# Kernel tuning notes

Hardware: AMD Instinct MI355X
Metric: run time of the kernel (lower is better)

## Reference

```python
import jax, jax.numpy as jnp
import numpy as np

N_HEADS = 16


def setup_inputs() -> dict:
    key = jax.random.key(0)
    k1, k2, k3 = jax.random.split(key, 3)
    B, S, D = 2, 2048, 1024
    x = jax.random.normal(k1, (B, S, D), dtype=jnp.float32)
    # causal mask: 1 = keep, 0 = masked (module does masked_fill(mask == 0, -inf))
    mask = jnp.broadcast_to(jnp.tril(jnp.ones((S, S), dtype=jnp.int32)), (B, S, S))
    # torch Linear(bias=False) weights, stored transposed so y = x @ W
    w_qkv = jax.random.normal(k2, (D, 3 * D), dtype=jnp.float32) * (1.0 / np.sqrt(D))
    w_out = jax.random.normal(k3, (D, D), dtype=jnp.float32) * (1.0 / np.sqrt(D))
    return {"x": x, "mask": mask, "w_qkv": w_qkv, "w_out": w_out}


def reference(x, mask, w_qkv, w_out):
    B, S, D = x.shape
    H = N_HEADS
    dh = D // H
    scale = 1.0 / np.sqrt(dh)

    qkv = x @ w_qkv                                   # [B,S,3D]
    qkv = qkv.reshape(B, S, 3, H, dh)
    qkv = jnp.transpose(qkv, (2, 0, 3, 1, 4))         # [3,B,H,S,dh]
    q, k, v = qkv[0], qkv[1], qkv[2]

    scores = jnp.einsum("bhqd,bhkd->bhqk", q, k) * scale   # [B,H,S,S]
    scores = jnp.where(mask[:, None, :, :] == 0, -jnp.inf, scores)
    attn = jax.nn.softmax(scores, axis=-1)            # dropout = identity (eval)

    out = jnp.einsum("bhqk,bhkd->bhqd", attn, v)      # [B,H,S,dh]
    out = jnp.transpose(out, (0, 2, 1, 3)).reshape(B, S, D)
    return out @ w_out
```

## Files before the change

### kernel.cpp

```cpp
#include <hip/hip_runtime.h>

typedef unsigned short u16;
typedef unsigned int u32;
typedef u16 u16x8 __attribute__((ext_vector_type(8)));
typedef u16 u16x4 __attribute__((ext_vector_type(4)));
typedef u32 u32x4 __attribute__((ext_vector_type(4)));
typedef __bf16 bf16x8 __attribute__((ext_vector_type(8)));
typedef float f32x4 __attribute__((ext_vector_type(4)));
typedef float f32x16 __attribute__((ext_vector_type(16)));


static __device__ __forceinline__ u16 bf16_rn(float f) {
    union { float f; u32 u; } a; a.f = f;
    u32 u = a.u;
    return (u16)((u + 0x7FFFu + ((u >> 16) & 1u)) >> 16);
}

static __device__ __forceinline__ bf16x8 as_bf(u16x8 v) {
    return __builtin_bit_cast(bf16x8, v);
}

static __device__ __forceinline__ u32 cvt_pk_bf16(float lo, float hi) {
    u32 r;
    asm("v_cvt_pk_bf16_f32 %0, %1, %2" : "=v"(r) : "v"(lo), "v"(hi));
    return r;
}

static __device__ __forceinline__ void glds16(const u16* g, u16* lds) {
    __builtin_amdgcn_global_load_lds(
        (const __attribute__((address_space(1))) void*)g,
        (__attribute__((address_space(3))) void*)lds, 16, 0, 0);
}


__global__ void k_cvt(const float* __restrict__ src, u16* __restrict__ dst, int n8) {
    int i = blockIdx.x * blockDim.x + threadIdx.x;
    if (i >= n8) return;
    const float4* s = (const float4*)src + (size_t)i * 2;
    float4 a = s[0], b = s[1];
    u16x8 v;
    v[0] = bf16_rn(a.x); v[1] = bf16_rn(a.y); v[2] = bf16_rn(a.z); v[3] = bf16_rn(a.w);
    v[4] = bf16_rn(b.x); v[5] = bf16_rn(b.y); v[6] = bf16_rn(b.z); v[7] = bf16_rn(b.w);
    *(u16x8*)(dst + (size_t)i * 8) = v;
}


__global__ void k_tr_cvt(const float* __restrict__ src, u16* __restrict__ dst,
                         int R, int C) {
    __shared__ float t[32][33];
    const int bx = blockIdx.x * 32, by = blockIdx.y * 32;
    const int tx = threadIdx.x, ty = threadIdx.y;
#pragma unroll
    for (int j = 0; j < 32; j += 8)
        t[ty + j][tx] = src[(size_t)(by + ty + j) * C + bx + tx];
    __syncthreads();
#pragma unroll
    for (int j = 0; j < 32; j += 8)
        dst[(size_t)(bx + ty + j) * R + by + tx] = bf16_rn(t[tx][ty + j]);
}


template <int MODE>
__launch_bounds__(256, 2)
__global__ void k_gemm(const u16* __restrict__ A, const u16* __restrict__ Bt,
                       void* __restrict__ outp, int M, int N, int K) {
    __shared__ __align__(16) u16 As[2][128 * 32];
    __shared__ __align__(16) u16 Bs[2][128 * 32];
    const int tid = threadIdx.x;
    const int l = tid & 63, wv = tid >> 6;
    const int wr = wv >> 1, wc = wv & 1;
    const int l15 = l & 15, lg = l >> 4;
    const int m0 = blockIdx.y * 128, n0 = blockIdx.x * 128;
    const int NT = K >> 5;

    const f32x4 fzero = {0.f, 0.f, 0.f, 0.f};
    f32x4 acc[4][4];
#pragma unroll
    for (int m = 0; m < 4; m++)
#pragma unroll
        for (int n = 0; n < 4; n++) acc[m][n] = fzero;

    const int grow0 = wv * 32 + (l >> 2);
    const int gcol = (l & 3) * 8;

    auto stage = [&](int buf, int kt) {
        const size_t ko = (size_t)kt * 32 + gcol;
        glds16(A  + (size_t)(m0 + grow0) * K + ko,      &As[buf][wv * 1024]);
        glds16(A  + (size_t)(m0 + grow0 + 16) * K + ko, &As[buf][wv * 1024 + 512]);
        glds16(Bt + (size_t)(n0 + grow0) * K + ko,      &Bs[buf][wv * 1024]);
        glds16(Bt + (size_t)(n0 + grow0 + 16) * K + ko, &Bs[buf][wv * 1024 + 512]);
    };

    stage(0, 0);
    int cur = 0;
    for (int kt = 0; kt < NT; ++kt) {
        if (kt + 1 < NT) {
            stage(cur ^ 1, kt + 1);
            asm volatile("s_waitcnt vmcnt(4)" ::: "memory");
        } else {
            asm volatile("s_waitcnt vmcnt(0)" ::: "memory");
        }
        __builtin_amdgcn_s_barrier();
        u16x8 af[4], bfv[4];
#pragma unroll
        for (int m = 0; m < 4; m++)
            af[m] = *(const u16x8*)(&As[cur][(wr * 64 + m * 16 + l15) * 32 + lg * 8]);
#pragma unroll
        for (int n = 0; n < 4; n++)
            bfv[n] = *(const u16x8*)(&Bs[cur][(wc * 64 + n * 16 + l15) * 32 + lg * 8]);
#pragma unroll
        for (int m = 0; m < 4; m++)
#pragma unroll
            for (int n = 0; n < 4; n++)
                acc[m][n] = __builtin_amdgcn_mfma_f32_16x16x32_bf16(
                    as_bf(af[m]), as_bf(bfv[n]), acc[m][n], 0, 0, 0);
        __builtin_amdgcn_s_barrier();
        cur ^= 1;
    }

    if (MODE == 0) {
        u16* qkv = (u16*)outp;
#pragma unroll
        for (int m = 0; m < 4; m++) {
            const int rb = m0 + wr * 64 + m * 16 + lg * 4;
#pragma unroll
            for (int n = 0; n < 4; n++) {
                const int c = n0 + wc * 64 + n * 16;
                const int t = c >> 10, h = (c >> 6) & 15, d0 = (c & 63) + l15;
                const float scl = (t == 0) ? 0.18033688011112042f : 1.0f;
#pragma unroll
                for (int i = 0; i < 4; i++) {
                    const int r = rb + i;
                    const int b = r >> 11, s = r & 2047;
                    qkv[((((size_t)t * 2 + b) * 16 + h) * 2048 + s) * 64 + d0] =
                        bf16_rn(acc[m][n][i] * scl);
                }
            }
        }
    } else {
        float* O = (float*)outp;
#pragma unroll
        for (int m = 0; m < 4; m++) {
            const int rb = m0 + wr * 64 + m * 16 + lg * 4;
#pragma unroll
            for (int n = 0; n < 4; n++) {
                const int c = n0 + wc * 64 + n * 16 + l15;
#pragma unroll
                for (int i = 0; i < 4; i++)
                    O[(size_t)(rb + i) * N + c] = acc[m][n][i];
            }
        }
    }
}


__launch_bounds__(256, 3)
__global__ void k_attn(const u16* __restrict__ qkv, u16* __restrict__ ab) {
    __shared__ __align__(16) char arena[4][9216];
    __shared__ float MLs[4][64];
    const int tid = threadIdx.x, l = tid & 63, wv = tid >> 6;
    const int q = l & 31, h = l >> 5;
    const int bid = blockIdx.x;
    const int bh = bid & 31;
    const int pp = bid >> 5;
    const int b = bh >> 4, hd = bh & 15;
    const size_t plane = (size_t)2048 * 64;
    const u16* Qg = qkv + ((size_t)(0 + b) * 16 + hd) * plane;
    const u16* Kg = qkv + ((size_t)(2 + b) * 16 + hd) * plane;
    const u16* Vg = qkv + ((size_t)(4 + b) * 16 + hd) * plane;
    u16* VT = (u16*)arena[wv];

    const int g = l & 7, qd = l >> 3;
    const u16* Kbase = Kg + (size_t)q * 64 + 8 * h;
    const u16* Vbase = Vg + (size_t)(8 * qd) * 64 + 8 * g;
    const int Fq0 = 8 * (q >> 3) + ((q & 7) ^ ((q >> 3) & 7));
    const int d1 = q + 32;
    const int Fq1 = 8 * (d1 >> 3) + ((d1 & 7) ^ ((d1 >> 3) & 7));
    const u16* vr0 = VT + Fq0 * 72 + 8 * h;
    const u16* vr1 = VT + Fq1 * 72 + 8 * h;
    const float FIXM = 12.0f;

    for (int ph = 0; ph < 4; ++ph) {
        const int pr = (ph & 2) ? pp + 16 : pp;
        const int qt = (ph & 1) ? 63 - pr : pr;
        const int q0 = qt * 32, qg = q0 + q;
        const int n64 = (qt >> 1) + 1;

        u16x8 qf[4];
#pragma unroll
        for (int s = 0; s < 4; ++s)
            qf[s] = *(const u16x8*)(Qg + (size_t)(q0 + q) * 64 + s * 16 + 8 * h);

        f32x16 oacc0 = 0, oacc1 = 0;
        float l_run = 0.f;

        u16x8 vK[8];
        if (wv < n64) {
#pragma unroll
            for (int s = 0; s < 4; ++s) {
                vK[s]     = *(const u16x8*)(Kbase + (size_t)(wv * 64) * 64 + s * 16);
                vK[4 + s] = *(const u16x8*)(Kbase + (size_t)(wv * 64 + 32) * 64 + s * 16);
            }
        }

        for (int t = wv; t < n64; t += 4) {
            const int kv0 = t * 64;
            u16x8 vV[8];
#pragma unroll
            for (int j = 0; j < 8; ++j)
                vV[j] = *(const u16x8*)(Vbase + (size_t)(kv0 + j) * 64);
            f32x16 sa = 0, sb = 0;
            __builtin_amdgcn_s_setprio(1);
#pragma unroll
            for (int s = 0; s < 4; ++s)
                sa = __builtin_amdgcn_mfma_f32_32x32x16_bf16(as_bf(vK[s]), as_bf(qf[s]), sa, 0, 0, 0);
#pragma unroll
            for (int s = 0; s < 4; ++s)
                sb = __builtin_amdgcn_mfma_f32_32x32x16_bf16(as_bf(vK[4 + s]), as_bf(qf[s]), sb, 0, 0, 0);
            __builtin_amdgcn_s_setprio(0);
#pragma unroll
            for (int j = 0; j < 8; ++j) {
                u16x8 col;
#pragma unroll
                for (int r = 0; r < 8; ++r) col[r] = vV[r][j];
                *(u16x8*)(VT + (size_t)(8 * g + (j ^ g)) * 72 + 8 * qd) = col;
            }
            if (t + 4 < n64) {
#pragma unroll
                for (int s = 0; s < 4; ++s) {
                    vK[s]     = *(const u16x8*)(Kbase + (size_t)((t + 4) * 64) * 64 + s * 16);
                    vK[4 + s] = *(const u16x8*)(Kbase + (size_t)((t + 4) * 64 + 32) * 64 + s * 16);
                }
            }
            if (t == n64 - 1) {
#pragma unroll
                for (int r = 0; r < 16; ++r) {
                    const int kg = kv0 + (r & 3) + 8 * (r >> 2) + 4 * h;
                    if (kg > qg) sa[r] = -__builtin_inff();
                    if (kg + 32 > qg) sb[r] = -__builtin_inff();
                }
            }
#pragma unroll
            for (int r = 0; r < 16; ++r) sa[r] = exp2f(sa[r] - FIXM);
#pragma unroll
            for (int r = 0; r < 16; ++r) sb[r] = exp2f(sb[r] - FIXM);
            float ts[8];
#pragma unroll
            for (int i = 0; i < 8; ++i)
                ts[i] = (sa[i] + sa[i + 8]) + (sb[i] + sb[i + 8]);
#pragma unroll
            for (int i = 0; i < 4; ++i) ts[i] += ts[i + 4];
            l_run += (ts[0] + ts[2]) + (ts[1] + ts[3]);
            u32 pk[16];
#pragma unroll
            for (int i = 0; i < 8; ++i) pk[i]     = cvt_pk_bf16(sa[2 * i], sa[2 * i + 1]);
#pragma unroll
            for (int i = 0; i < 8; ++i) pk[8 + i] = cvt_pk_bf16(sb[2 * i], sb[2 * i + 1]);
#pragma unroll
            for (int ks = 0; ks < 4; ++ks) {
                const int base = (ks >> 1) * 8 + 4 * (ks & 1);
                const u32 o0 = pk[base], o1 = pk[base + 1], o2 = pk[base + 2], o3 = pk[base + 3];
                const u32 sd0 = h ? o0 : o2, sd1 = h ? o1 : o3;
                const u32 r0 = (u32)__shfl_xor((int)sd0, 32);
                const u32 r1 = (u32)__shfl_xor((int)sd1, 32);
                const u32 w0 = h ? r0 : o0, w1 = h ? r1 : o1;
                const u32 w2 = h ? o2 : r0, w3 = h ? o3 : r1;
                const u16x8 pb = __builtin_bit_cast(u16x8, (u32x4){w0, w1, w2, w3});
                const u16x8 va0 = *(const u16x8*)(vr0 + ks * 16);
                const u16x8 va1 = *(const u16x8*)(vr1 + ks * 16);
                __builtin_amdgcn_s_setprio(1);
                oacc0 = __builtin_amdgcn_mfma_f32_32x32x16_bf16(as_bf(va0), as_bf(pb), oacc0, 0, 0, 0);
                oacc1 = __builtin_amdgcn_mfma_f32_32x32x16_bf16(as_bf(va1), as_bf(pb), oacc1, 0, 0, 0);
                __builtin_amdgcn_s_setprio(0);
            }
        }
        asm volatile("" ::: "memory");
        float* Op = (float*)arena[wv];
#pragma unroll
        for (int r = 0; r < 16; ++r) {
            const int dr = (r & 3) + 8 * (r >> 2) + 4 * h;
            Op[q * 64 + ((dr + 2 * q) & 63)]      = oacc0[r];
            Op[q * 64 + ((dr + 32 + 2 * q) & 63)] = oacc1[r];
        }
        MLs[wv][l] = l_run;
        __syncthreads();
        const int tq = tid >> 3, dblk = (tid & 7) * 8;
        float L = 0.f;
#pragma unroll
        for (int w = 0; w < 4; ++w) L += MLs[w][tq] + MLs[w][32 + tq];
        const float inv = 1.f / L;
        u16x8 outv;
#pragma unroll
        for (int j = 0; j < 8; ++j) {
            const int d = dblk + j;
            float acc = 0.f;
#pragma unroll
            for (int w = 0; w < 4; ++w)
                acc += ((const float*)arena[w])[tq * 64 + ((d + 2 * tq) & 63)];
            outv[j] = bf16_rn(acc * inv);
        }
        *(u16x8*)(ab + (size_t)(b * 2048 + q0 + tq) * 1024 + hd * 64 + dblk) = outv;
        __syncthreads();
    }
}


extern "C" void kernel_launch(void* const* d_in, const int* in_sizes, int n_in,
                              void* d_out, int out_size, void* d_ws, size_t ws_size,
                              hipStream_t stream) {
    const float* x     = (const float*)d_in[0];
    const float* w_qkv = (const float*)d_in[2];
    const float* w_out = (const float*)d_in[3];
    float* out = (float*)d_out;
    u16* ws = (u16*)d_ws;

    u16* xb    = ws;
    u16* wqkvT = ws + 4194304;
    u16* woutT = ws + 7340032;
    u16* qkvb  = ws + 8388608;
    u16* abuf  = ws;

    k_cvt<<<2048, 256, 0, stream>>>(x, xb, 524288);
    k_tr_cvt<<<dim3(96, 32), dim3(32, 8), 0, stream>>>(w_qkv, wqkvT, 1024, 3072);
    k_tr_cvt<<<dim3(32, 32), dim3(32, 8), 0, stream>>>(w_out, woutT, 1024, 1024);
    k_gemm<0><<<dim3(24, 32), 256, 0, stream>>>(xb, wqkvT, qkvb, 4096, 3072, 1024);
    k_attn<<<512, 256, 0, stream>>>(qkvb, abuf);
    k_gemm<1><<<dim3(8, 32), 256, 0, stream>>>(abuf, woutT, out, 4096, 1024, 1024);
}
```

Before: 133.9 us.

## Split attention KV tile into two 32-key halves to interleave softmax and MFMA

The inner attention loop now processes each 64-key tile as two 32-key halves. It computes scores, exp, bf16 packing and the PV MFMAs for the first half before issuing the QK MFMAs for the second half. V transposes and the K prefetch loads are also split and spread across the halves. The aim is to cut peak register pressure and let exp and conversion work overlap with matrix instructions. The risk is more serialized dependencies within a wave, plus extra half-width LDS writes.

Result: no change. 136.0 us (+1.6%).

```diff
diff --git a/kernel.cpp b/kernel.cpp
--- a/kernel.cpp
+++ b/kernel.cpp
@@ -205,61 +205,61 @@
 
         for (int t = wv; t < n64; t += 4) {
             const int kv0 = t * 64;
-            u16x8 vV[8];
-#pragma unroll
-            for (int j = 0; j < 8; ++j)
-                vV[j] = *(const u16x8*)(Vbase + (size_t)(kv0 + j) * 64);
-            f32x16 sa = 0, sb = 0;
+            const bool diag = (t == n64 - 1);
+            const bool more = (t + 4 < n64);
+            u16x4 cA[4];
+            u16x8 vVa[4];
+#pragma unroll
+            for (int j = 0; j < 4; ++j)
+                vVa[j] = *(const u16x8*)(Vbase + (size_t)(kv0 + j) * 64);
+            f32x16 sa = 0;
             __builtin_amdgcn_s_setprio(1);
 #pragma unroll
             for (int s = 0; s < 4; ++s)
                 sa = __builtin_amdgcn_mfma_f32_32x32x16_bf16(as_bf(vK[s]), as_bf(qf[s]), sa, 0, 0, 0);
-#pragma unroll
-            for (int s = 0; s < 4; ++s)
-                sb = __builtin_amdgcn_mfma_f32_32x32x16_bf16(as_bf(vK[4 + s]), as_bf(qf[s]), sb, 0, 0, 0);
             __builtin_amdgcn_s_setprio(0);
+            u16x8 vVb[4];
+#pragma unroll
+            for (int j = 0; j < 4; ++j)
+                vVb[j] = *(const u16x8*)(Vbase + (size_t)(kv0 + 4 + j) * 64);
 #pragma unroll
             for (int j = 0; j < 8; ++j) {
-                u16x8 col;
-#pragma unroll
-                for (int r = 0; r < 8; ++r) col[r] = vV[r][j];
-                *(u16x8*)(VT + (size_t)(8 * g + (j ^ g)) * 72 + 8 * qd) = col;
-            }
-            if (t + 4 < n64) {
-#pragma unroll
-                for (int s = 0; s < 4; ++s) {
-                    vK[s]     = *(const u16x8*)(Kbase + (size_t)((t + 4) * 64) * 64 + s * 16);
-                    vK[4 + s] = *(const u16x8*)(Kbase + (size_t)((t + 4) * 64 + 32) * 64 + s * 16);
-                }
-            }
-            if (t == n64 - 1) {
+                u16x4 col = { vVa[0][j], vVa[1][j], vVa[2][j], vVa[3][j] };
+                *(u16x4*)(VT + (size_t)(8 * g + (j ^ g)) * 72 + 8 * qd) = col;
+            }
+            if (diag) {
 #pragma unroll
                 for (int r = 0; r < 16; ++r) {
                     const int kg = kv0 + (r & 3) + 8 * (r >> 2) + 4 * h;
                     if (kg > qg) sa[r] = -__builtin_inff();
-                    if (kg + 32 > qg) sb[r] = -__builtin_inff();
                 }
             }
 #pragma unroll
             for (int r = 0; r < 16; ++r) sa[r] = exp2f(sa[r] - FIXM);
-#pragma unroll
-            for (int r = 0; r < 16; ++r) sb[r] = exp2f(sb[r] - FIXM);
-            float ts[8];
-#pragma unroll
-            for (int i = 0; i < 8; ++i)
-                ts[i] = (sa[i] + sa[i + 8]) + (sb[i] + sb[i + 8]);
-#pragma unroll
-            for (int i = 0; i < 4; ++i) ts[i] += ts[i + 4];
-            l_run += (ts[0] + ts[2]) + (ts[1] + ts[3]);
-            u32 pk[16];
-#pragma unroll
-            for (int i = 0; i < 8; ++i) pk[i]     = cvt_pk_bf16(sa[2 * i], sa[2 * i + 1]);
-#pragma unroll
-            for (int i = 0; i < 8; ++i) pk[8 + i] = cvt_pk_bf16(sb[2 * i], sb[2 * i + 1]);
-#pragma unroll
-            for (int ks = 0; ks < 4; ++ks) {
-                const int base = (ks >> 1) * 8 + 4 * (ks & 1);
-                const u32 o0 = pk[base], o1 = pk[base + 1], o2 = pk[base + 2], o3 = pk[base + 3];
+            {
+                float ts[4];
+#pragma unroll
+                for (int i = 0; i < 4; ++i)
+                    ts[i] = (sa[i] + sa[i + 4]) + (sa[i + 8] + sa[i + 12]);
+                l_run += (ts[0] + ts[2]) + (ts[1] + ts[3]);
+            }
+            u32 pka[8];
+#pragma unroll
+            for (int i = 0; i < 8; ++i) pka[i] = cvt_pk_bf16(sa[2 * i], sa[2 * i + 1]);
+#pragma unroll
+            for (int j = 0; j < 8; ++j) {
+                u16x4 col = { vVb[0][j], vVb[1][j], vVb[2][j], vVb[3][j] };
+                *(u16x4*)(VT + (size_t)(8 * g + (j ^ g)) * 72 + 8 * qd + 4) = col;
+            }
+            if (more) {
+#pragma unroll
+                for (int s = 0; s < 4; ++s)
+                    vK[s] = *(const u16x8*)(Kbase + (size_t)((t + 4) * 64) * 64 + s * 16);
+            }
+#pragma unroll
+            for (int ks = 0; ks < 2; ++ks) {
+                const u32 o0 = pka[4 * ks], o1 = pka[4 * ks + 1];
+                const u32 o2 = pka[4 * ks + 2], o3 = pka[4 * ks + 3];
                 const u32 sd0 = h ? o0 : o2, sd1 = h ? o1 : o3;
                 const u32 r0 = (u32)__shfl_xor((int)sd0, 32);
                 const u32 r1 = (u32)__shfl_xor((int)sd1, 32);
@@ -273,6 +273,54 @@
                 oacc1 = __builtin_amdgcn_mfma_f32_32x32x16_bf16(as_bf(va1), as_bf(pb), oacc1, 0, 0, 0);
                 __builtin_amdgcn_s_setprio(0);
             }
+            f32x16 sb = 0;
+            __builtin_amdgcn_s_setprio(1);
+#pragma unroll
+            for (int s = 0; s < 4; ++s)
+                sb = __builtin_amdgcn_mfma_f32_32x32x16_bf16(as_bf(vK[4 + s]), as_bf(qf[s]), sb, 0, 0, 0);
+            __builtin_amdgcn_s_setprio(0);
+            if (diag) {
+#pragma unroll
+                for (int r = 0; r < 16; ++r) {
+                    const int kg = kv0 + 32 + (r & 3) + 8 * (r >> 2) + 4 * h;
+                    if (kg > qg) sb[r] = -__builtin_inff();
+                }
+            }
+#pragma unroll
+            for (int r = 0; r < 16; ++r) sb[r] = exp2f(sb[r] - FIXM);
+            {
+                float ts[4];
+#pragma unroll
+                for (int i = 0; i < 4; ++i)
+                    ts[i] = (sb[i] + sb[i + 4]) + (sb[i + 8] + sb[i + 12]);
+                l_run += (ts[0] + ts[2]) + (ts[1] + ts[3]);
+            }
+            u32 pkb[8];
+#pragma unroll
+            for (int i = 0; i < 8; ++i) pkb[i] = cvt_pk_bf16(sb[2 * i], sb[2 * i + 1]);
+            if (more) {
+#pragma unroll
+                for (int s = 0; s < 4; ++s)
+                    vK[4 + s] = *(const u16x8*)(Kbase + (size_t)((t + 4) * 64 + 32) * 64 + s * 16);
+            }
+#pragma unroll
+            for (int ks = 0; ks < 2; ++ks) {
+                const u32 o0 = pkb[4 * ks], o1 = pkb[4 * ks + 1];
+                const u32 o2 = pkb[4 * ks + 2], o3 = pkb[4 * ks + 3];
+                const u32 sd0 = h ? o0 : o2, sd1 = h ? o1 : o3;
+                const u32 r0 = (u32)__shfl_xor((int)sd0, 32);
+                const u32 r1 = (u32)__shfl_xor((int)sd1, 32);
+                const u32 w0 = h ? r0 : o0, w1 = h ? r1 : o1;
+                const u32 w2 = h ? o2 : r0, w3 = h ? o3 : r1;
+                const u16x8 pb = __builtin_bit_cast(u16x8, (u32x4){w0, w1, w2, w3});
+                const u16x8 va0 = *(const u16x8*)(vr0 + (2 + ks) * 16);
+                const u16x8 va1 = *(const u16x8*)(vr1 + (2 + ks) * 16);
+                __builtin_amdgcn_s_setprio(1);
+                oacc0 = __builtin_amdgcn_mfma_f32_32x32x16_bf16(as_bf(va0), as_bf(pb), oacc0, 0, 0, 0);
+                oacc1 = __builtin_amdgcn_mfma_f32_32x32x16_bf16(as_bf(va1), as_bf(pb), oacc1, 0, 0, 0);
+                __builtin_amdgcn_s_setprio(0);
+            }
+            (void)cA;
         }
         asm volatile("" ::: "memory");
         float* Op = (float*)arena[wv];
```

## Process two adjacent query tiles per pass to reuse K and V loads

Applied to the files above, without the earlier changes.

The attention kernel now handles a pair of adjacent 32-row query tiles (A and B) in each of two passes, instead of one tile in each of four passes. Each K fragment and each transposed V tile is loaded and staged once and then used for both query tiles, which halves the global and LDS traffic per unit of MFMA work. The extra accumulators and Q fragments raise register pressure, so launch bounds drop from 3 to 2 blocks per SM, which reduces occupancy. Causal work balance is kept by pairing tiles from both ends of the sequence.

New measurement: 138.5 us. 3.4% more time.

```diff
diff --git a/kernel.cpp b/kernel.cpp
--- a/kernel.cpp
+++ b/kernel.cpp
@@ -154,7 +154,7 @@
 }
 
 
-__launch_bounds__(256, 3)
+__launch_bounds__(256, 2)
 __global__ void k_attn(const u16* __restrict__ qkv, u16* __restrict__ ab) {
     __shared__ __align__(16) char arena[4][9216];
     __shared__ float MLs[4][64];
@@ -162,7 +162,7 @@
     const int q = l & 31, h = l >> 5;
     const int bid = blockIdx.x;
     const int bh = bid & 31;
-    const int pp = bid >> 5;
+    const int kk = bid >> 5;
     const int b = bh >> 4, hd = bh & 15;
     const size_t plane = (size_t)2048 * 64;
     const u16* Qg = qkv + ((size_t)(0 + b) * 16 + hd) * plane;
@@ -180,19 +180,21 @@
     const u16* vr1 = VT + Fq1 * 72 + 8 * h;
     const float FIXM = 12.0f;
 
-    for (int ph = 0; ph < 4; ++ph) {
-        const int pr = (ph & 2) ? pp + 16 : pp;
-        const int qt = (ph & 1) ? 63 - pr : pr;
-        const int q0 = qt * 32, qg = q0 + q;
-        const int n64 = (qt >> 1) + 1;
-
-        u16x8 qf[4];
-#pragma unroll
-        for (int s = 0; s < 4; ++s)
-            qf[s] = *(const u16x8*)(Qg + (size_t)(q0 + q) * 64 + s * 16 + 8 * h);
-
-        f32x16 oacc0 = 0, oacc1 = 0;
-        float l_run = 0.f;
+    for (int half = 0; half < 2; ++half) {
+        const int qtA = half ? 62 - 2 * kk : 2 * kk;
+        const int q0A = qtA * 32, q0B = q0A + 32;
+        const int qgA = q0A + q, qgB = q0B + q;
+        const int n64 = half ? 32 - kk : kk + 1;
+
+        u16x8 qfA[4], qfB[4];
+#pragma unroll
+        for (int s = 0; s < 4; ++s) {
+            qfA[s] = *(const u16x8*)(Qg + (size_t)(q0A + q) * 64 + s * 16 + 8 * h);
+            qfB[s] = *(const u16x8*)(Qg + (size_t)(q0B + q) * 64 + s * 16 + 8 * h);
+        }
+
+        f32x16 oA0 = 0, oA1 = 0, oB0 = 0, oB1 = 0;
+        float lA = 0.f, lB = 0.f;
 
         u16x8 vK[8];
         if (wv < n64) {
@@ -205,18 +207,19 @@
 
         for (int t = wv; t < n64; t += 4) {
             const int kv0 = t * 64;
+            const bool diag = (t == n64 - 1);
             u16x8 vV[8];
 #pragma unroll
             for (int j = 0; j < 8; ++j)
                 vV[j] = *(const u16x8*)(Vbase + (size_t)(kv0 + j) * 64);
-            f32x16 sa = 0, sb = 0;
+            f32x16 saA = 0, sbA = 0;
             __builtin_amdgcn_s_setprio(1);
 #pragma unroll
             for (int s = 0; s < 4; ++s)
-                sa = __builtin_amdgcn_mfma_f32_32x32x16_bf16(as_bf(vK[s]), as_bf(qf[s]), sa, 0, 0, 0);
+                saA = __builtin_amdgcn_mfma_f32_32x32x16_bf16(as_bf(vK[s]), as_bf(qfA[s]), saA, 0, 0, 0);
 #pragma unroll
             for (int s = 0; s < 4; ++s)
-                sb = __builtin_amdgcn_mfma_f32_32x32x16_bf16(as_bf(vK[4 + s]), as_bf(qf[s]), sb, 0, 0, 0);
+                sbA = __builtin_amdgcn_mfma_f32_32x32x16_bf16(as_bf(vK[4 + s]), as_bf(qfA[s]), sbA, 0, 0, 0);
             __builtin_amdgcn_s_setprio(0);
 #pragma unroll
             for (int j = 0; j < 8; ++j) {
@@ -225,6 +228,15 @@
                 for (int r = 0; r < 8; ++r) col[r] = vV[r][j];
                 *(u16x8*)(VT + (size_t)(8 * g + (j ^ g)) * 72 + 8 * qd) = col;
             }
+            f32x16 saB = 0, sbB = 0;
+            __builtin_amdgcn_s_setprio(1);
+#pragma unroll
+            for (int s = 0; s < 4; ++s)
+                saB = __builtin_amdgcn_mfma_f32_32x32x16_bf16(as_bf(vK[s]), as_bf(qfB[s]), saB, 0, 0, 0);
+#pragma unroll
+            for (int s = 0; s < 4; ++s)
+                sbB = __builtin_amdgcn_mfma_f32_32x32x16_bf16(as_bf(vK[4 + s]), as_bf(qfB[s]), sbB, 0, 0, 0);
+            __builtin_amdgcn_s_setprio(0);
             if (t + 4 < n64) {
 #pragma unroll
                 for (int s = 0; s < 4; ++s) {
@@ -232,75 +244,131 @@
                     vK[4 + s] = *(const u16x8*)(Kbase + (size_t)((t + 4) * 64 + 32) * 64 + s * 16);
                 }
             }
-            if (t == n64 - 1) {
+            if (diag) {
 #pragma unroll
                 for (int r = 0; r < 16; ++r) {
                     const int kg = kv0 + (r & 3) + 8 * (r >> 2) + 4 * h;
-                    if (kg > qg) sa[r] = -__builtin_inff();
-                    if (kg + 32 > qg) sb[r] = -__builtin_inff();
-                }
-            }
-#pragma unroll
-            for (int r = 0; r < 16; ++r) sa[r] = exp2f(sa[r] - FIXM);
-#pragma unroll
-            for (int r = 0; r < 16; ++r) sb[r] = exp2f(sb[r] - FIXM);
-            float ts[8];
-#pragma unroll
-            for (int i = 0; i < 8; ++i)
-                ts[i] = (sa[i] + sa[i + 8]) + (sb[i] + sb[i + 8]);
-#pragma unroll
-            for (int i = 0; i < 4; ++i) ts[i] += ts[i + 4];
-            l_run += (ts[0] + ts[2]) + (ts[1] + ts[3]);
-            u32 pk[16];
-#pragma unroll
-            for (int i = 0; i < 8; ++i) pk[i]     = cvt_pk_bf16(sa[2 * i], sa[2 * i + 1]);
-#pragma unroll
-            for (int i = 0; i < 8; ++i) pk[8 + i] = cvt_pk_bf16(sb[2 * i], sb[2 * i + 1]);
-#pragma unroll
-            for (int ks = 0; ks < 4; ++ks) {
-                const int base = (ks >> 1) * 8 + 4 * (ks & 1);
-                const u32 o0 = pk[base], o1 = pk[base + 1], o2 = pk[base + 2], o3 = pk[base + 3];
-                const u32 sd0 = h ? o0 : o2, sd1 = h ? o1 : o3;
-                const u32 r0 = (u32)__shfl_xor((int)sd0, 32);
-                const u32 r1 = (u32)__shfl_xor((int)sd1, 32);
-                const u32 w0 = h ? r0 : o0, w1 = h ? r1 : o1;
-                const u32 w2 = h ? o2 : r0, w3 = h ? o3 : r1;
-                const u16x8 pb = __builtin_bit_cast(u16x8, (u32x4){w0, w1, w2, w3});
-                const u16x8 va0 = *(const u16x8*)(vr0 + ks * 16);
-                const u16x8 va1 = *(const u16x8*)(vr1 + ks * 16);
-                __builtin_amdgcn_s_setprio(1);
-                oacc0 = __builtin_amdgcn_mfma_f32_32x32x16_bf16(as_bf(va0), as_bf(pb), oacc0, 0, 0, 0);
-                oacc1 = __builtin_amdgcn_mfma_f32_32x32x16_bf16(as_bf(va1), as_bf(pb), oacc1, 0, 0, 0);
-                __builtin_amdgcn_s_setprio(0);
-            }
-        }
-        asm volatile("" ::: "memory");
-        float* Op = (float*)arena[wv];
-#pragma unroll
-        for (int r = 0; r < 16; ++r) {
-            const int dr = (r & 3) + 8 * (r >> 2) + 4 * h;
-            Op[q * 64 + ((dr + 2 * q) & 63)]      = oacc0[r];
-            Op[q * 64 + ((dr + 32 + 2 * q) & 63)] = oacc1[r];
-        }
-        MLs[wv][l] = l_run;
-        __syncthreads();
-        const int tq = tid >> 3, dblk = (tid & 7) * 8;
-        float L = 0.f;
-#pragma unroll
-        for (int w = 0; w < 4; ++w) L += MLs[w][tq] + MLs[w][32 + tq];
-        const float inv = 1.f / L;
-        u16x8 outv;
-#pragma unroll
-        for (int j = 0; j < 8; ++j) {
-            const int d = dblk + j;
-            float acc = 0.f;
-#pragma unroll
-            for (int w = 0; w < 4; ++w)
-                acc += ((const float*)arena[w])[tq * 64 + ((d + 2 * tq) & 63)];
-            outv[j] = bf16_rn(acc * inv);
-        }
-        *(u16x8*)(ab + (size_t)(b * 2048 + q0 + tq) * 1024 + hd * 64 + dblk) = outv;
-        __syncthreads();
+                    if (kg > qgA) saA[r] = -__builtin_inff();
+                    if (kg + 32 > qgA) sbA[r] = -__builtin_inff();
+                }
+            }
+#pragma unroll
+            for (int r = 0; r < 16; ++r) saA[r] = exp2f(saA[r] - FIXM);
+#pragma unroll
+            for (int r = 0; r < 16; ++r) sbA[r] = exp2f(sbA[r] - FIXM);
+            {
+                float ts[8];
+#pragma unroll
+                for (int i = 0; i < 8; ++i)
+                    ts[i] = (saA[i] + saA[i + 8]) + (sbA[i] + sbA[i + 8]);
+#pragma unroll
+                for (int i = 0; i < 4; ++i) ts[i] += ts[i + 4];
+                lA += (ts[0] + ts[2]) + (ts[1] + ts[3]);
+            }
+            {
+                u32 pk[16];
+#pragma unroll
+                for (int i = 0; i < 8; ++i) pk[i]     = cvt_pk_bf16(saA[2 * i], saA[2 * i + 1]);
+#pragma unroll
+                for (int i = 0; i < 8; ++i) pk[8 + i] = cvt_pk_bf16(sbA[2 * i], sbA[2 * i + 1]);
+#pragma unroll
+                for (int ks = 0; ks < 4; ++ks) {
+                    const int base = (ks >> 1) * 8 + 4 * (ks & 1);
+                    const u32 o0 = pk[base], o1 = pk[base + 1], o2 = pk[base + 2], o3 = pk[base + 3];
+                    const u32 sd0 = h ? o0 : o2, sd1 = h ? o1 : o3;
+                    const u32 r0 = (u32)__shfl_xor((int)sd0, 32);
+                    const u32 r1 = (u32)__shfl_xor((int)sd1, 32);
+                    const u32 w0 = h ? r0 : o0, w1 = h ? r1 : o1;
+                    const u32 w2 = h ? o2 : r0, w3 = h ? o3 : r1;
+                    const u16x8 pb = __builtin_bit_cast(u16x8, (u32x4){w0, w1, w2, w3});
+                    const u16x8 va0 = *(const u16x8*)(vr0 + ks * 16);
+                    const u16x8 va1 = *(const u16x8*)(vr1 + ks * 16);
+                    __builtin_amdgcn_s_setprio(1);
+                    oA0 = __builtin_amdgcn_mfma_f32_32x32x16_bf16(as_bf(va0), as_bf(pb), oA0, 0, 0, 0);
+                    oA1 = __builtin_amdgcn_mfma_f32_32x32x16_bf16(as_bf(va1), as_bf(pb), oA1, 0, 0, 0);
+                    __builtin_amdgcn_s_setprio(0);
+                }
+            }
+            if (diag) {
+#pragma unroll
+                for (int r = 0; r < 16; ++r) {
+                    const int kg = kv0 + (r & 3) + 8 * (r >> 2) + 4 * h;
+                    if (kg > qgB) saB[r] = -__builtin_inff();
+                    if (kg + 32 > qgB) sbB[r] = -__builtin_inff();
+                }
+            }
+#pragma unroll
+            for (int r = 0; r < 16; ++r) saB[r] = exp2f(saB[r] - FIXM);
+#pragma unroll
+            for (int r = 0; r < 16; ++r) sbB[r] = exp2f(sbB[r] - FIXM);
+            {
+                float ts[8];
+#pragma unroll
+                for (int i = 0; i < 8; ++i)
+                    ts[i] = (saB[i] + saB[i + 8]) + (sbB[i] + sbB[i + 8]);
+#pragma unroll
+                for (int i = 0; i < 4; ++i) ts[i] += ts[i + 4];
+                lB += (ts[0] + ts[2]) + (ts[1] + ts[3]);
+            }
+            {
+                u32 pk[16];
+#pragma unroll
+                for (int i = 0; i < 8; ++i) pk[i]     = cvt_pk_bf16(saB[2 * i], saB[2 * i + 1]);
+#pragma unroll
+                for (int i = 0; i < 8; ++i) pk[8 + i] = cvt_pk_bf16(sbB[2 * i], sbB[2 * i + 1]);
+#pragma unroll
+                for (int ks = 0; ks < 4; ++ks) {
+                    const int base = (ks >> 1) * 8 + 4 * (ks & 1);
+                    const u32 o0 = pk[base], o1 = pk[base + 1], o2 = pk[base + 2], o3 = pk[base + 3];
+                    const u32 sd0 = h ? o0 : o2, sd1 = h ? o1 : o3;
+                    const u32 r0 = (u32)__shfl_xor((int)sd0, 32);
+                    const u32 r1 = (u32)__shfl_xor((int)sd1, 32);
+                    const u32 w0 = h ? r0 : o0, w1 = h ? r1 : o1;
+                    const u32 w2 = h ? o2 : r0, w3 = h ? o3 : r1;
+                    const u16x8 pb = __builtin_bit_cast(u16x8, (u32x4){w0, w1, w2, w3});
+                    const u16x8 va0 = *(const u16x8*)(vr0 + ks * 16);
+                    const u16x8 va1 = *(const u16x8*)(vr1 + ks * 16);
+                    __builtin_amdgcn_s_setprio(1);
+                    oB0 = __builtin_amdgcn_mfma_f32_32x32x16_bf16(as_bf(va0), as_bf(pb), oB0, 0, 0, 0);
+                    oB1 = __builtin_amdgcn_mfma_f32_32x32x16_bf16(as_bf(va1), as_bf(pb), oB1, 0, 0, 0);
+                    __builtin_amdgcn_s_setprio(0);
+                }
+            }
+        }
+#pragma unroll
+        for (int tile = 0; tile < 2; ++tile) {
+            const f32x16& e0 = tile ? oB0 : oA0;
+            const f32x16& e1 = tile ? oB1 : oA1;
+            const float lr = tile ? lB : lA;
+            const int q0 = tile ? q0B : q0A;
+            asm volatile("" ::: "memory");
+            float* Op = (float*)arena[wv];
+#pragma unroll
+            for (int r = 0; r < 16; ++r) {
+                const int dr = (r & 3) + 8 * (r >> 2) + 4 * h;
+                Op[q * 64 + ((dr + 2 * q) & 63)]      = e0[r];
+                Op[q * 64 + ((dr + 32 + 2 * q) & 63)] = e1[r];
+            }
+            MLs[wv][l] = lr;
+            __syncthreads();
+            const int tq = tid >> 3, dblk = (tid & 7) * 8;
+            float L = 0.f;
+#pragma unroll
+            for (int w = 0; w < 4; ++w) L += MLs[w][tq] + MLs[w][32 + tq];
+            const float inv = 1.f / L;
+            u16x8 outv;
+#pragma unroll
+            for (int j = 0; j < 8; ++j) {
+                const int d = dblk + j;
+                float acc = 0.f;
+#pragma unroll
+                for (int w = 0; w < 4; ++w)
+                    acc += ((const float*)arena[w])[tq * 64 + ((d + 2 * tq) & 63)];
+                outv[j] = bf16_rn(acc * inv);
+            }
+            *(u16x8*)(ab + (size_t)(b * 2048 + q0 + tq) * 1024 + hd * 64 + dblk) = outv;
+            __syncthreads();
+        }
     }
 }
 
```
